# Performance work log

Measured on AMD Instinct MI355X. Metric: run time of the kernel, lower is better.

## Reference

```python
import jax, jax.numpy as jnp
import numpy as np

B, E, D, H, A = 65536, 16, 256, 64, 18  # batch, n_subpolicies, emb_dim, hidden, n_actions


def setup_inputs() -> dict:
    key = jax.random.key(0)
    ks = jax.random.split(key, 16)
    s = lambda k, sh: jax.random.normal(k, sh, dtype=jnp.float32) * 0.05
    return dict(
        obs=s(ks[0], (B, D)),
        h=s(ks[1], (B, D)),
        c=s(ks[2], (B, D)),
        idxs=jax.random.randint(ks[3], (B,), 0, E, dtype=jnp.int32),
        # Observer: LSTMCell(D, D) params (torch layout: [4D, D] with i,f,g,o gate order)
        W_ih=s(ks[4], (4 * D, D)), W_hh=s(ks[5], (4 * D, D)),
        b_ih=s(ks[6], (4 * D,)), b_hh=s(ks[7], (4 * D,)),
        # Stacked SubPolicy actor params: Linear(D,64)-Tanh-Linear(64,A)
        Wa1=s(ks[8], (E, D, H)), ba1=s(ks[9], (E, H)),
        Wa2=s(ks[10], (E, H, A)), ba2=s(ks[11], (E, A)),
        # Stacked SubPolicy critic params: Linear(D,64)-Tanh-Linear(64,1)
        Wc1=s(ks[12], (E, D, H)), bc1=s(ks[13], (E, H)),
        Wc2=s(ks[14], (E, H, 1)), bc2=s(ks[15], (E, 1)),
    )


def reference(obs, h, c, idxs, W_ih, W_hh, b_ih, b_hh,
              Wa1, ba1, Wa2, ba2, Wc1, bc1, Wc2, bc2):
    # ---- Observer: single LSTMCell step ----
    gates = obs @ W_ih.T + b_ih + h @ W_hh.T + b_hh          # [B, 4D]
    gi, gf, gg, go = jnp.split(gates, 4, axis=1)
    i = jax.nn.sigmoid(gi); f = jax.nn.sigmoid(gf); o = jax.nn.sigmoid(go)
    c_new = f * c + i * jnp.tanh(gg)                          # [B, D]
    h_new = o * jnp.tanh(c_new)                               # [B, D]

    # ---- Expert dispatch: evaluate all tiny subpolicy MLPs, select per sample ----
    # (mathematically identical to the per-sample routing loop in forward_sub)
    ha = jnp.tanh(jnp.einsum('bd,edh->beh', h_new, Wa1) + ba1)        # [B, E, H]
    logits_all = jnp.einsum('beh,eha->bea', ha, Wa2) + ba2            # [B, E, A]
    hc = jnp.tanh(jnp.einsum('bd,edh->beh', h_new, Wc1) + bc1)        # [B, E, H]
    vals_all = (jnp.einsum('beh,eho->beo', hc, Wc2) + bc2)[..., 0]    # [B, E]

    b = jnp.arange(h_new.shape[0])
    logits = logits_all[b, idxs]                                       # [B, A]
    values = vals_all[b, idxs]                                         # [B]
    return (h_new, c_new, logits, values)
```

## Files before the change

kernel.cpp:

```cpp
#include <hip/hip_runtime.h>
#include <hip/hip_bf16.h>
#include <math.h>

#define NB 65536
#define ND 256
#define NE 16
#define NH 64
#define NA 18

typedef __bf16 bf16;
typedef __bf16 bf16x4 __attribute__((ext_vector_type(4)));
typedef __bf16 bf16x8 __attribute__((ext_vector_type(8)));
typedef float  f32x4  __attribute__((ext_vector_type(4)));

#define OFF_WCAT 0u
#define OFF_BCAT 1048576u
#define OFF_PW1  1052672u
#define OFF_B1   2101248u
#define OFF_CUR  2109440u
#define OFF_PERM 2109504u

__device__ __forceinline__ float rcp_(float x) { return __builtin_amdgcn_rcpf(x); }
__device__ __forceinline__ float sigm_(float x) { return rcp_(1.f + __expf(-x)); }
__device__ __forceinline__ float tanh_(float x) {
    float cl = fminf(fmaxf(x, -15.f), 15.f);
    float e = __expf(2.f * cl);
    return (e - 1.f) * rcp_(e + 1.f);
}

__device__ __forceinline__ void gl2lds16(const void* g, void* l) {
    __builtin_amdgcn_global_load_lds(
        (const __attribute__((address_space(1))) unsigned int*)g,
        (__attribute__((address_space(3))) unsigned int*)l, 16, 0, 0);
}

__global__ void k_prep1(const float* __restrict__ W_ih, const float* __restrict__ W_hh,
                        const float* __restrict__ b_ih, const float* __restrict__ b_hh,
                        char* __restrict__ ws) {
    int t = blockIdx.x * 256 + threadIdx.x;
    int kstep = t >> 13, rem = t & 8191;
    int cb = rem >> 11, u = rem & 2047;
    int hi = u >> 8, lo = u & 255;
    int kf = hi >> 2, g = hi & 3;
    int colw = lo >> 2, lk = lo & 3;
    int col = g * 256 + cb * 64 + colw;
    int k0 = kstep * 64 + (kf * 4 + lk) * 8;
    const float* src = (k0 < 256) ? (W_ih + (size_t)col * 256 + k0)
                                  : (W_hh + (size_t)col * 256 + (k0 - 256));
    float4 v0 = *(const float4*)(src);
    float4 v1 = *(const float4*)(src + 4);
    bf16x8 o;
    o[0] = (bf16)v0.x; o[1] = (bf16)v0.y; o[2] = (bf16)v0.z; o[3] = (bf16)v0.w;
    o[4] = (bf16)v1.x; o[5] = (bf16)v1.y; o[6] = (bf16)v1.z; o[7] = (bf16)v1.w;
    *(bf16x8*)((bf16*)(ws + OFF_WCAT) + (size_t)t * 8) = o;
    if (t < 1024) ((float*)(ws + OFF_BCAT))[t] = b_ih[t] + b_hh[t];
    if (t < 16)   ((int*)(ws + OFF_CUR))[t] = t * 65536;
}

__global__ void k_prep2(const float* __restrict__ Wa1, const float* __restrict__ Wc1,
                        const float* __restrict__ ba1, const float* __restrict__ bc1,
                        char* __restrict__ ws) {
    int t = blockIdx.x * 256 + threadIdx.x;
    bf16* PW1 = (bf16*)(ws + OFF_PW1);
    int col = t & 127, kc = (t >> 7) & 31, e = t >> 12;
    bf16x8 o;
#pragma unroll
    for (int j = 0; j < 8; ++j) {
        int k = kc * 8 + j;
        float v = (col < 64) ? Wa1[((size_t)e * 256 + k) * 64 + col]
                             : Wc1[((size_t)e * 256 + k) * 64 + (col - 64)];
        o[j] = (bf16)v;
    }
    *(bf16x8*)(PW1 + (((size_t)e * 32 + kc) * 128 + col) * 8) = o;
    if (t < 2048) {
        int e2 = t >> 7, c = t & 127;
        ((float*)(ws + OFF_B1))[t] = (c < 64) ? ba1[e2 * 64 + c] : bc1[e2 * 64 + (c - 64)];
    }
}

__global__ void k_scatter(const int* __restrict__ idxs, char* __restrict__ ws) {
    __shared__ int lh[16], lbase[16];
    int t = threadIdx.x;
    int i = blockIdx.x * 256 + t;
    if (t < 16) lh[t] = 0;
    __syncthreads();
    int e = idxs[i];
    int r = atomicAdd(&lh[e], 1);
    __syncthreads();
    int* cur = (int*)(ws + OFF_CUR);
    if (t < 16) lbase[t] = atomicAdd(&cur[t], lh[t]);
    __syncthreads();
    ((int*)(ws + OFF_PERM))[lbase[e] + r] = i;
}

__global__ __launch_bounds__(256, 2) void k_lstm(
    const float* __restrict__ obs, const float* __restrict__ hin,
    const float* __restrict__ cin, const float* __restrict__ bcat,
    const char* __restrict__ wcat,
    float* __restrict__ hout, float* __restrict__ cout) {
    __shared__ alignas(16) char Abuf[2][8192];
    __shared__ alignas(16) char Bbuf[2][32768];
    const int tid  = threadIdx.x;
    const int w = tid >> 6, lane = tid & 63;
    const int lr = lane & 15, lk = lane >> 4;
    const int rb = blockIdx.x & 1023, cb = blockIdx.x >> 10;
    const int row0 = rb * 64;
    const int colc = cb * 64 + w * 16 + lr;
    const int srw = tid >> 3, sj = tid & 7;

    const char* WcatBlk = wcat + (size_t)cb * 32768;
    const float* baseO0 = obs + (size_t)(row0 + srw) * 256 + sj * 8;
    const float* baseH0 = hin + (size_t)(row0 + srw) * 256 + sj * 8;

    int offE[4], offO[4];
#pragma unroll
    for (int m = 0; m < 4; ++m) {
        int R = m * 16 + lr;
        offE[m] = lk * 1024 + ((R ^ lk) * 16);
        offO[m] = (lk + 4) * 1024 + ((R ^ (lk + 4)) * 16);
    }
    const int bBase = (w * 16 + lr) * 64 + lk * 16;

    f32x4 acc[4][4];
#pragma unroll
    for (int m = 0; m < 4; ++m)
#pragma unroll
        for (int g = 0; g < 4; ++g)
#pragma unroll
            for (int r = 0; r < 4; ++r) acc[m][g][r] = 0.f;

#define STAGE_B(bi, ks)                                                      \
    {                                                                        \
        const char* srcB_ = WcatBlk + (size_t)(ks) * 131072;                 \
        _Pragma("unroll")                                                    \
        for (int i_ = 0; i_ < 8; ++i_) {                                     \
            int so_ = (w * 8 + i_) * 1024;                                   \
            gl2lds16(srcB_ + so_ + lane * 16, &Bbuf[bi][so_]);               \
        }                                                                    \
    }
#define LOAD_A(ks)                                                           \
    {                                                                        \
        const float* s0_ = ((ks) < 4) ? (baseO0 + (ks) * 64)                 \
                                      : (baseH0 + ((ks) - 4) * 64);          \
        na0 = *(const float4*)(s0_);                                         \
        na1 = *(const float4*)(s0_ + 4);                                     \
        nb0 = *(const float4*)(s0_ + 32 * 256);                              \
        nb1 = *(const float4*)(s0_ + 32 * 256 + 4);                          \
    }
#define WRITE_A(bi)                                                          \
    {                                                                        \
        bf16x8 oa_, ob_;                                                     \
        oa_[0] = (bf16)na0.x; oa_[1] = (bf16)na0.y; oa_[2] = (bf16)na0.z;    \
        oa_[3] = (bf16)na0.w; oa_[4] = (bf16)na1.x; oa_[5] = (bf16)na1.y;    \
        oa_[6] = (bf16)na1.z; oa_[7] = (bf16)na1.w;                          \
        ob_[0] = (bf16)nb0.x; ob_[1] = (bf16)nb0.y; ob_[2] = (bf16)nb0.z;    \
        ob_[3] = (bf16)nb0.w; ob_[4] = (bf16)nb1.x; ob_[5] = (bf16)nb1.y;    \
        ob_[6] = (bf16)nb1.z; ob_[7] = (bf16)nb1.w;                          \
        *(bf16x8*)(&Abuf[bi][sj * 1024 + ((srw ^ sj) * 16)]) = oa_;          \
        *(bf16x8*)(&Abuf[bi][sj * 1024 + (((srw + 32) ^ sj) * 16)]) = ob_;   \
    }

    {
        float4 na0, na1, nb0, nb1;
        STAGE_B(0, 0);
        LOAD_A(0);
        WRITE_A(0);
    }
    __syncthreads();

    float cpre[16];

#pragma unroll
    for (int t = 0; t < 8; ++t) {
        const int cur = t & 1;
        float4 na0, na1, nb0, nb1;
        if (t < 7) {
            STAGE_B(cur ^ 1, t + 1);
            LOAD_A(t + 1);
        } else {
#pragma unroll
            for (int m = 0; m < 4; ++m)
#pragma unroll
                for (int r = 0; r < 4; ++r)
                    cpre[m * 4 + r] = cin[(size_t)(row0 + m * 16 + lk * 4 + r) * 256 + colc];
        }
#pragma unroll
        for (int kf = 0; kf < 2; ++kf) {
            const char* Ab = Abuf[cur];
            const int* offA = kf ? offO : offE;
            bf16x8 a0 = *(const bf16x8*)(Ab + offA[0]);
            bf16x8 a1 = *(const bf16x8*)(Ab + offA[1]);
            bf16x8 a2 = *(const bf16x8*)(Ab + offA[2]);
            bf16x8 a3 = *(const bf16x8*)(Ab + offA[3]);
            const char* Bb = Bbuf[cur] + kf * 16384 + bBase;
            bf16x8 b0 = *(const bf16x8*)(Bb);
            bf16x8 b1 = *(const bf16x8*)(Bb + 4096);
            bf16x8 b2 = *(const bf16x8*)(Bb + 8192);
            bf16x8 b3 = *(const bf16x8*)(Bb + 12288);
            acc[0][0] = __builtin_amdgcn_mfma_f32_16x16x32_bf16(a0, b0, acc[0][0], 0, 0, 0);
            acc[1][0] = __builtin_amdgcn_mfma_f32_16x16x32_bf16(a1, b0, acc[1][0], 0, 0, 0);
            acc[2][0] = __builtin_amdgcn_mfma_f32_16x16x32_bf16(a2, b0, acc[2][0], 0, 0, 0);
            acc[3][0] = __builtin_amdgcn_mfma_f32_16x16x32_bf16(a3, b0, acc[3][0], 0, 0, 0);
            acc[0][1] = __builtin_amdgcn_mfma_f32_16x16x32_bf16(a0, b1, acc[0][1], 0, 0, 0);
            acc[1][1] = __builtin_amdgcn_mfma_f32_16x16x32_bf16(a1, b1, acc[1][1], 0, 0, 0);
            acc[2][1] = __builtin_amdgcn_mfma_f32_16x16x32_bf16(a2, b1, acc[2][1], 0, 0, 0);
            acc[3][1] = __builtin_amdgcn_mfma_f32_16x16x32_bf16(a3, b1, acc[3][1], 0, 0, 0);
            acc[0][2] = __builtin_amdgcn_mfma_f32_16x16x32_bf16(a0, b2, acc[0][2], 0, 0, 0);
            acc[1][2] = __builtin_amdgcn_mfma_f32_16x16x32_bf16(a1, b2, acc[1][2], 0, 0, 0);
            acc[2][2] = __builtin_amdgcn_mfma_f32_16x16x32_bf16(a2, b2, acc[2][2], 0, 0, 0);
            acc[3][2] = __builtin_amdgcn_mfma_f32_16x16x32_bf16(a3, b2, acc[3][2], 0, 0, 0);
            acc[0][3] = __builtin_amdgcn_mfma_f32_16x16x32_bf16(a0, b3, acc[0][3], 0, 0, 0);
            acc[1][3] = __builtin_amdgcn_mfma_f32_16x16x32_bf16(a1, b3, acc[1][3], 0, 0, 0);
            acc[2][3] = __builtin_amdgcn_mfma_f32_16x16x32_bf16(a2, b3, acc[2][3], 0, 0, 0);
            acc[3][3] = __builtin_amdgcn_mfma_f32_16x16x32_bf16(a3, b3, acc[3][3], 0, 0, 0);
        }
        if (t < 7) WRITE_A(cur ^ 1);
        __syncthreads();
    }
#undef STAGE_B
#undef LOAD_A
#undef WRITE_A

    float bi = bcat[colc], bf_ = bcat[256 + colc], bg = bcat[512 + colc], bo = bcat[768 + colc];
#pragma unroll
    for (int m = 0; m < 4; ++m) {
#pragma unroll
        for (int r = 0; r < 4; ++r) {
            int row = row0 + m * 16 + lk * 4 + r;
            float gi = acc[m][0][r] + bi;
            float gf = acc[m][1][r] + bf_;
            float gg = acc[m][2][r] + bg;
            float go = acc[m][3][r] + bo;
            float iv = sigm_(gi), fv = sigm_(gf), gv = tanh_(gg), ov = sigm_(go);
            float cn = fv * cpre[m * 4 + r] + iv * gv;
            float hn = ov * tanh_(cn);
            cout[(size_t)row * 256 + colc] = cn;
            hout[(size_t)row * 256 + colc] = hn;
        }
    }
}

__global__ __launch_bounds__(256) void k_expert(
    const float* __restrict__ Wa2, const float* __restrict__ ba2,
    const float* __restrict__ Wc2, const float* __restrict__ bc2,
    char* __restrict__ ws, const float* __restrict__ hsrc,
    float* __restrict__ lout, float* __restrict__ vout) {
    const int e = blockIdx.y;
    const int* cur = (const int*)(ws + OFF_CUR);
    int cnt = cur[e] - e * 65536;
    int r0 = blockIdx.x * 64;
    if (r0 >= cnt) return;
    int nr = min(64, cnt - r0);
    const int* permE = (const int*)(ws + OFF_PERM) + (size_t)e * 65536 + r0;

    __shared__ int rows_s[64];
    __shared__ alignas(16) char smem[128 * 66 * 4];
    bf16*  Alds = (bf16*)smem;
    float* haF  = (float*)smem;

    int t = threadIdx.x;
    if (t < 64) rows_s[t] = permE[(t < nr) ? t : 0];
    __syncthreads();

    {
        int rowi = t >> 2, q = t & 3;
        const float* hp = hsrc + (size_t)rows_s[rowi] * 256;
#pragma unroll
        for (int s = 0; s < 8; ++s) {
            int kc = s * 4 + q;
            float4 v0 = *(const float4*)(hp + kc * 8);
            float4 v1 = *(const float4*)(hp + kc * 8 + 4);
            bf16x8 o;
            o[0] = (bf16)v0.x; o[1] = (bf16)v0.y; o[2] = (bf16)v0.z; o[3] = (bf16)v0.w;
            o[4] = (bf16)v1.x; o[5] = (bf16)v1.y; o[6] = (bf16)v1.z; o[7] = (bf16)v1.w;
            *(bf16x8*)(Alds + ((size_t)kc * 64 + rowi) * 8) = o;
        }
    }
    __syncthreads();

    const bf16* PW1 = (const bf16*)(ws + OFF_PW1) + (size_t)e * 32 * 128 * 8;
    const float* b1 = (const float*)(ws + OFF_B1) + e * 128;
    int wave = t >> 6, lane = t & 63, lr = lane & 15, lk = lane >> 4;

    f32x4 acc[4][2];
#pragma unroll
    for (int m = 0; m < 4; ++m)
#pragma unroll
        for (int n = 0; n < 2; ++n)
#pragma unroll
            for (int r = 0; r < 4; ++r) acc[m][n][r] = 0.f;

#pragma unroll
    for (int kf = 0; kf < 8; ++kf) {
        bf16x8 a[4], bb[2];
#pragma unroll
        for (int m = 0; m < 4; ++m)
            a[m] = *(const bf16x8*)(Alds + (((kf * 4 + lk) * 64) + (m * 16 + lr)) * 8);
#pragma unroll
        for (int n = 0; n < 2; ++n) {
            int colh = wave * 32 + n * 16 + lr;
            int kc = kf * 4 + lk;
            bb[n] = *(const bf16x8*)(PW1 + ((size_t)kc * 128 + colh) * 8);
        }
#pragma unroll
        for (int m = 0; m < 4; ++m)
#pragma unroll
            for (int n = 0; n < 2; ++n)
                acc[m][n] = __builtin_amdgcn_mfma_f32_16x16x32_bf16(a[m], bb[n], acc[m][n], 0, 0, 0);
    }
    __syncthreads();

#pragma unroll
    for (int m = 0; m < 4; ++m)
#pragma unroll
        for (int n = 0; n < 2; ++n) {
            int colh = wave * 32 + n * 16 + lr;
            float bbv = b1[colh];
#pragma unroll
            for (int r = 0; r < 4; ++r) {
                int row = m * 16 + lk * 4 + r;
                haF[colh * 66 + row] = tanh_(acc[m][n][r] + bbv);
            }
        }
    __syncthreads();

    int row = t & 63;
    int grow = rows_s[row];
    bool valid = row < nr;
#pragma unroll
    for (int p = 0; p < 5; ++p) {
        int aI = p * 4 + (t >> 6);
        if (aI < NA) {
            float s = ba2[e * NA + aI];
            for (int hh = 0; hh < 64; ++hh)
                s += haF[hh * 66 + row] * Wa2[((size_t)e * 64 + hh) * NA + aI];
            if (valid) lout[(size_t)grow * NA + aI] = s;
        }
    }
    if (t < 64) {
        float s = bc2[e];
        for (int hh = 0; hh < 64; ++hh)
            s += haF[(64 + hh) * 66 + row] * Wc2[e * 64 + hh];
        if (valid) vout[grow] = s;
    }
}

extern "C" void kernel_launch(void* const* d_in, const int* in_sizes, int n_in,
                              void* d_out, int out_size, void* d_ws, size_t ws_size,
                              hipStream_t stream) {
    const float* obs  = (const float*)d_in[0];
    const float* h    = (const float*)d_in[1];
    const float* c    = (const float*)d_in[2];
    const int*   idxs = (const int*)d_in[3];
    const float* W_ih = (const float*)d_in[4];
    const float* W_hh = (const float*)d_in[5];
    const float* b_ih = (const float*)d_in[6];
    const float* b_hh = (const float*)d_in[7];
    const float* Wa1  = (const float*)d_in[8];
    const float* ba1  = (const float*)d_in[9];
    const float* Wa2  = (const float*)d_in[10];
    const float* ba2  = (const float*)d_in[11];
    const float* Wc1  = (const float*)d_in[12];
    const float* bc1  = (const float*)d_in[13];
    const float* Wc2  = (const float*)d_in[14];
    const float* bc2  = (const float*)d_in[15];

    float* out  = (float*)d_out;
    float* hout = out;
    float* cout = out + (size_t)NB * ND;
    float* lout = out + (size_t)2 * NB * ND;
    float* vout = lout + (size_t)NB * NA;
    char* ws = (char*)d_ws;

    k_prep1<<<dim3(256), dim3(256), 0, stream>>>(W_ih, W_hh, b_ih, b_hh, ws);
    k_prep2<<<dim3(256), dim3(256), 0, stream>>>(Wa1, Wc1, ba1, bc1, ws);
    k_scatter<<<dim3(256), dim3(256), 0, stream>>>(idxs, ws);
    k_lstm<<<dim3(4096), dim3(256), 0, stream>>>(
        obs, h, c, (const float*)(ws + OFF_BCAT), (const char*)(ws + OFF_WCAT), hout, cout);
    k_expert<<<dim3(1024, 16), dim3(256), 0, stream>>>(
        Wa2, ba2, Wc2, bc2, ws, hout, lout, vout);
}
```

Baseline: 222.8 us.

## Swizzle LSTM weight LDS layout, reorder blocks, prefetch A two steps ahead

The LSTM GEMM kernel gets three changes. The packed weight layout and the B-fragment LDS read address now use an XOR swizzle, to avoid LDS bank conflicts on B reads. The grid mapping is flipped so the four column blocks of the same row block run adjacently, which lets them share obs/h rows in cache. Activation loads are double-buffered in registers two k-steps ahead, the c prefetch moves earlier, and the final barrier is dropped; this raises register pressure at launch_bounds(256,2).

```diff
diff --git a/kernel.cpp b/kernel.cpp
--- a/kernel.cpp
+++ b/kernel.cpp
@@ -38,13 +38,12 @@
                         const float* __restrict__ b_ih, const float* __restrict__ b_hh,
                         char* __restrict__ ws) {
     int t = blockIdx.x * 256 + threadIdx.x;
-    int kstep = t >> 13, rem = t & 8191;
-    int cb = rem >> 11, u = rem & 2047;
-    int hi = u >> 8, lo = u & 255;
-    int kf = hi >> 2, g = hi & 3;
-    int colw = lo >> 2, lk = lo & 3;
-    int col = g * 256 + cb * 64 + colw;
-    int k0 = kstep * 64 + (kf * 4 + lk) * 8;
+    int kstep = t >> 13;
+    int cb    = (t >> 11) & 3;
+    int idx   = t & 2047;
+    int kf = idx >> 10, g = (idx >> 8) & 3, lk = (idx >> 6) & 3, u = idx & 63;
+    int col = g * 256 + cb * 64 + (u ^ lk);
+    int k0  = kstep * 64 + (kf * 4 + lk) * 8;
     const float* src = (k0 < 256) ? (W_ih + (size_t)col * 256 + k0)
                                   : (W_hh + (size_t)col * 256 + (k0 - 256));
     float4 v0 = *(const float4*)(src);
@@ -103,7 +102,7 @@
     const int tid  = threadIdx.x;
     const int w = tid >> 6, lane = tid & 63;
     const int lr = lane & 15, lk = lane >> 4;
-    const int rb = blockIdx.x & 1023, cb = blockIdx.x >> 10;
+    const int rb = blockIdx.x >> 2, cb = blockIdx.x & 3;
     const int row0 = rb * 64;
     const int colc = cb * 64 + w * 16 + lr;
     const int srw = tid >> 3, sj = tid & 7;
@@ -119,7 +118,7 @@
         offE[m] = lk * 1024 + ((R ^ lk) * 16);
         offO[m] = (lk + 4) * 1024 + ((R ^ (lk + 4)) * 16);
     }
-    const int bBase = (w * 16 + lr) * 64 + lk * 16;
+    const int bBase = lk * 1024 + (((w * 16 + lr) ^ lk) * 16);
 
     f32x4 acc[4][4];
 #pragma unroll
@@ -138,88 +137,98 @@
             gl2lds16(srcB_ + so_ + lane * 16, &Bbuf[bi][so_]);               \
         }                                                                    \
     }
-#define LOAD_A(ks)                                                           \
+#define LOAD_A(ks, d0, d1, d2, d3)                                           \
     {                                                                        \
         const float* s0_ = ((ks) < 4) ? (baseO0 + (ks) * 64)                 \
                                       : (baseH0 + ((ks) - 4) * 64);          \
-        na0 = *(const float4*)(s0_);                                         \
-        na1 = *(const float4*)(s0_ + 4);                                     \
-        nb0 = *(const float4*)(s0_ + 32 * 256);                              \
-        nb1 = *(const float4*)(s0_ + 32 * 256 + 4);                          \
-    }
-#define WRITE_A(bi)                                                          \
+        d0 = *(const float4*)(s0_);                                          \
+        d1 = *(const float4*)(s0_ + 4);                                      \
+        d2 = *(const float4*)(s0_ + 32 * 256);                               \
+        d3 = *(const float4*)(s0_ + 32 * 256 + 4);                           \
+    }
+#define WRITE_A(bi, d0, d1, d2, d3)                                          \
     {                                                                        \
         bf16x8 oa_, ob_;                                                     \
-        oa_[0] = (bf16)na0.x; oa_[1] = (bf16)na0.y; oa_[2] = (bf16)na0.z;    \
-        oa_[3] = (bf16)na0.w; oa_[4] = (bf16)na1.x; oa_[5] = (bf16)na1.y;    \
-        oa_[6] = (bf16)na1.z; oa_[7] = (bf16)na1.w;                          \
-        ob_[0] = (bf16)nb0.x; ob_[1] = (bf16)nb0.y; ob_[2] = (bf16)nb0.z;    \
-        ob_[3] = (bf16)nb0.w; ob_[4] = (bf16)nb1.x; ob_[5] = (bf16)nb1.y;    \
-        ob_[6] = (bf16)nb1.z; ob_[7] = (bf16)nb1.w;                          \
+        oa_[0] = (bf16)d0.x; oa_[1] = (bf16)d0.y; oa_[2] = (bf16)d0.z;       \
+        oa_[3] = (bf16)d0.w; oa_[4] = (bf16)d1.x; oa_[5] = (bf16)d1.y;       \
+        oa_[6] = (bf16)d1.z; oa_[7] = (bf16)d1.w;                            \
+        ob_[0] = (bf16)d2.x; ob_[1] = (bf16)d2.y; ob_[2] = (bf16)d2.z;       \
+        ob_[3] = (bf16)d2.w; ob_[4] = (bf16)d3.x; ob_[5] = (bf16)d3.y;       \
+        ob_[6] = (bf16)d3.z; ob_[7] = (bf16)d3.w;                            \
         *(bf16x8*)(&Abuf[bi][sj * 1024 + ((srw ^ sj) * 16)]) = oa_;          \
         *(bf16x8*)(&Abuf[bi][sj * 1024 + (((srw + 32) ^ sj) * 16)]) = ob_;   \
     }
-
-    {
-        float4 na0, na1, nb0, nb1;
-        STAGE_B(0, 0);
-        LOAD_A(0);
-        WRITE_A(0);
-    }
-    __syncthreads();
-
+#define MFMA_STEP(cur)                                                       \
+    {                                                                        \
+        _Pragma("unroll")                                                    \
+        for (int kf = 0; kf < 2; ++kf) {                                     \
+            const char* Ab = Abuf[cur];                                      \
+            const int* offA = kf ? offO : offE;                              \
+            bf16x8 a0 = *(const bf16x8*)(Ab + offA[0]);                      \
+            bf16x8 a1 = *(const bf16x8*)(Ab + offA[1]);                      \
+            bf16x8 a2 = *(const bf16x8*)(Ab + offA[2]);                      \
+            bf16x8 a3 = *(const bf16x8*)(Ab + offA[3]);                      \
+            const char* Bb = Bbuf[cur] + kf * 16384 + bBase;                 \
+            bf16x8 b0 = *(const bf16x8*)(Bb);                                \
+            bf16x8 b1 = *(const bf16x8*)(Bb + 4096);                         \
+            bf16x8 b2 = *(const bf16x8*)(Bb + 8192);                         \
+            bf16x8 b3 = *(const bf16x8*)(Bb + 12288);                        \
+            acc[0][0] = __builtin_amdgcn_mfma_f32_16x16x32_bf16(a0, b0, acc[0][0], 0, 0, 0); \
+            acc[1][0] = __builtin_amdgcn_mfma_f32_16x16x32_bf16(a1, b0, acc[1][0], 0, 0, 0); \
+            acc[2][0] = __builtin_amdgcn_mfma_f32_16x16x32_bf16(a2, b0, acc[2][0], 0, 0, 0); \
+            acc[3][0] = __builtin_amdgcn_mfma_f32_16x16x32_bf16(a3, b0, acc[3][0], 0, 0, 0); \
+            acc[0][1] = __builtin_amdgcn_mfma_f32_16x16x32_bf16(a0, b1, acc[0][1], 0, 0, 0); \
+            acc[1][1] = __builtin_amdgcn_mfma_f32_16x16x32_bf16(a1, b1, acc[1][1], 0, 0, 0); \
+            acc[2][1] = __builtin_amdgcn_mfma_f32_16x16x32_bf16(a2, b1, acc[2][1], 0, 0, 0); \
+            acc[3][1] = __builtin_amdgcn_mfma_f32_16x16x32_bf16(a3, b1, acc[3][1], 0, 0, 0); \
+            acc[0][2] = __builtin_amdgcn_mfma_f32_16x16x32_bf16(a0, b2, acc[0][2], 0, 0, 0); \
+            acc[1][2] = __builtin_amdgcn_mfma_f32_16x16x32_bf16(a1, b2, acc[1][2], 0, 0, 0); \
+            acc[2][2] = __builtin_amdgcn_mfma_f32_16x16x32_bf16(a2, b2, acc[2][2], 0, 0, 0); \
+            acc[3][2] = __builtin_amdgcn_mfma_f32_16x16x32_bf16(a3, b2, acc[3][2], 0, 0, 0); \
+            acc[0][3] = __builtin_amdgcn_mfma_f32_16x16x32_bf16(a0, b3, acc[0][3], 0, 0, 0); \
+            acc[1][3] = __builtin_amdgcn_mfma_f32_16x16x32_bf16(a1, b3, acc[1][3], 0, 0, 0); \
+            acc[2][3] = __builtin_amdgcn_mfma_f32_16x16x32_bf16(a2, b3, acc[2][3], 0, 0, 0); \
+            acc[3][3] = __builtin_amdgcn_mfma_f32_16x16x32_bf16(a3, b3, acc[3][3], 0, 0, 0); \
+        }                                                                    \
+    }
+
+    float4 pA0, pA1, pA2, pA3;
+    float4 pB0, pB1, pB2, pB3;
     float cpre[16];
+
+    LOAD_A(0, pA0, pA1, pA2, pA3);
+    STAGE_B(0, 0);
+    WRITE_A(0, pA0, pA1, pA2, pA3);
+    LOAD_A(1, pA0, pA1, pA2, pA3);
+    __syncthreads();
 
 #pragma unroll
     for (int t = 0; t < 8; ++t) {
         const int cur = t & 1;
-        float4 na0, na1, nb0, nb1;
-        if (t < 7) {
-            STAGE_B(cur ^ 1, t + 1);
-            LOAD_A(t + 1);
+        if (t < 7) STAGE_B(cur ^ 1, t + 1);
+        if ((t & 1) == 0) {
+            if (t + 2 < 8) { LOAD_A(t + 2, pB0, pB1, pB2, pB3); }
         } else {
+            if (t + 2 < 8) { LOAD_A(t + 2, pA0, pA1, pA2, pA3); }
+        }
+        if (t == 6) {
 #pragma unroll
             for (int m = 0; m < 4; ++m)
 #pragma unroll
                 for (int r = 0; r < 4; ++r)
                     cpre[m * 4 + r] = cin[(size_t)(row0 + m * 16 + lk * 4 + r) * 256 + colc];
         }
-#pragma unroll
-        for (int kf = 0; kf < 2; ++kf) {
-            const char* Ab = Abuf[cur];
-            const int* offA = kf ? offO : offE;
-            bf16x8 a0 = *(const bf16x8*)(Ab + offA[0]);
-            bf16x8 a1 = *(const bf16x8*)(Ab + offA[1]);
-            bf16x8 a2 = *(const bf16x8*)(Ab + offA[2]);
-            bf16x8 a3 = *(const bf16x8*)(Ab + offA[3]);
-            const char* Bb = Bbuf[cur] + kf * 16384 + bBase;
-            bf16x8 b0 = *(const bf16x8*)(Bb);
-            bf16x8 b1 = *(const bf16x8*)(Bb + 4096);
-            bf16x8 b2 = *(const bf16x8*)(Bb + 8192);
-            bf16x8 b3 = *(const bf16x8*)(Bb + 12288);
-            acc[0][0] = __builtin_amdgcn_mfma_f32_16x16x32_bf16(a0, b0, acc[0][0], 0, 0, 0);
-            acc[1][0] = __builtin_amdgcn_mfma_f32_16x16x32_bf16(a1, b0, acc[1][0], 0, 0, 0);
-            acc[2][0] = __builtin_amdgcn_mfma_f32_16x16x32_bf16(a2, b0, acc[2][0], 0, 0, 0);
-            acc[3][0] = __builtin_amdgcn_mfma_f32_16x16x32_bf16(a3, b0, acc[3][0], 0, 0, 0);
-            acc[0][1] = __builtin_amdgcn_mfma_f32_16x16x32_bf16(a0, b1, acc[0][1], 0, 0, 0);
-            acc[1][1] = __builtin_amdgcn_mfma_f32_16x16x32_bf16(a1, b1, acc[1][1], 0, 0, 0);
-            acc[2][1] = __builtin_amdgcn_mfma_f32_16x16x32_bf16(a2, b1, acc[2][1], 0, 0, 0);
-            acc[3][1] = __builtin_amdgcn_mfma_f32_16x16x32_bf16(a3, b1, acc[3][1], 0, 0, 0);
-            acc[0][2] = __builtin_amdgcn_mfma_f32_16x16x32_bf16(a0, b2, acc[0][2], 0, 0, 0);
-            acc[1][2] = __builtin_amdgcn_mfma_f32_16x16x32_bf16(a1, b2, acc[1][2], 0, 0, 0);
-            acc[2][2] = __builtin_amdgcn_mfma_f32_16x16x32_bf16(a2, b2, acc[2][2], 0, 0, 0);
-            acc[3][2] = __builtin_amdgcn_mfma_f32_16x16x32_bf16(a3, b2, acc[3][2], 0, 0, 0);
-            acc[0][3] = __builtin_amdgcn_mfma_f32_16x16x32_bf16(a0, b3, acc[0][3], 0, 0, 0);
-            acc[1][3] = __builtin_amdgcn_mfma_f32_16x16x32_bf16(a1, b3, acc[1][3], 0, 0, 0);
-            acc[2][3] = __builtin_amdgcn_mfma_f32_16x16x32_bf16(a2, b3, acc[2][3], 0, 0, 0);
-            acc[3][3] = __builtin_amdgcn_mfma_f32_16x16x32_bf16(a3, b3, acc[3][3], 0, 0, 0);
-        }
-        if (t < 7) WRITE_A(cur ^ 1);
-        __syncthreads();
+        MFMA_STEP(cur);
+        if (t < 7) {
+            if ((t & 1) == 0) { WRITE_A(cur ^ 1, pA0, pA1, pA2, pA3); }
+            else              { WRITE_A(cur ^ 1, pB0, pB1, pB2, pB3); }
+            __syncthreads();
+        }
     }
 #undef STAGE_B
 #undef LOAD_A
 #undef WRITE_A
+#undef MFMA_STEP
 
     float bi = bcat[colc], bf_ = bcat[256 + colc], bg = bcat[512 + colc], bo = bcat[768 + colc];
 #pragma unroll
```

Measured after the change: 217.3 us. -2.5%, faster.
